# Kernel optimization log

Hardware: AMD Instinct MI355X
Metric: run time of the kernel (lower is better)

The kernel has to match this reference:

```python
import jax, jax.numpy as jnp
import numpy as np

DIM = 256
KEY_DIM = 16
NUM_HEADS = 8
ATTN_RATIO = 4
RES = (32, 32)
N = RES[0] * RES[1]            # 1024 tokens
D = ATTN_RATIO * KEY_DIM       # 64 per-head value dim
DH = D * NUM_HEADS             # 512
H_QKV = DH + 2 * KEY_DIM * NUM_HEADS  # 768
BATCH = 32
EPS = 1e-5


def _bias_idxs():
    # relative-position offset index table: idx[i,j] = |dr|*W + |dc| (bijective
    # over the res0*res1 unique abs-offset pairs, matching the gather structure)
    r = np.arange(RES[0])
    c = np.arange(RES[1])
    rr, cc = np.meshgrid(r, c, indexing='ij')
    pr = rr.reshape(-1)  # [N]
    pc = cc.reshape(-1)
    dr = np.abs(pr[:, None] - pr[None, :])
    dc = np.abs(pc[:, None] - pc[None, :])
    return jnp.asarray(dr * RES[1] + dc, dtype=jnp.int32)  # [N, N]


def setup_inputs() -> dict:
    key = jax.random.key(0)
    ks = jax.random.split(key, 8)
    s_in = 1.0 / np.sqrt(DIM)
    s_dh = 1.0 / np.sqrt(DH)
    return {
        'x': jax.random.normal(ks[0], (BATCH, N, DIM), jnp.float32),
        'norm_w': jnp.ones((DIM,), jnp.float32),
        'norm_b': jnp.zeros((DIM,), jnp.float32),
        'qkv_w': jax.random.normal(ks[1], (H_QKV, DIM), jnp.float32) * s_in,
        'qkv_b': jnp.zeros((H_QKV,), jnp.float32),
        'proj_w': jax.random.normal(ks[2], (DIM, DH), jnp.float32) * s_dh,
        'proj_b': jnp.zeros((DIM,), jnp.float32),
        'attn_biases': jax.random.normal(ks[3], (NUM_HEADS, RES[0] * RES[1]), jnp.float32) * 0.02,
        'bias_idxs': _bias_idxs(),
    }


def reference(x, norm_w, norm_b, qkv_w, qkv_b, proj_w, proj_b, attn_biases, bias_idxs):
    b, n, _ = x.shape
    scale = KEY_DIM ** -0.5
    # LayerNorm
    mu = jnp.mean(x, axis=-1, keepdims=True)
    var = jnp.mean(jnp.square(x - mu), axis=-1, keepdims=True)
    xn = (x - mu) * jax.lax.rsqrt(var + EPS) * norm_w + norm_b
    # fused qkv projection
    qkv = xn @ qkv_w.T + qkv_b                       # [b, n, H_QKV]
    qkv = qkv.reshape(b, n, NUM_HEADS, 2 * KEY_DIM + D)
    q = qkv[..., :KEY_DIM]                           # [b, n, h, k]
    k = qkv[..., KEY_DIM:2 * KEY_DIM]
    v = qkv[..., 2 * KEY_DIM:]                       # [b, n, h, d]
    # scores + gathered relative-position bias
    bias = attn_biases[:, bias_idxs]                 # [h, n, n]
    attn = jnp.einsum('bnhk,bmhk->bhnm', q, k) * scale + bias
    attn = jax.nn.softmax(attn, axis=-1)
    out = jnp.einsum('bhnm,bmhd->bnhd', attn, v).reshape(b, n, DH)
    return out @ proj_w.T + proj_b                   # [b, n, DIM]
```

## Files before the change

### kernel.cpp

```cpp
#include <hip/hip_runtime.h>
#include <hip/hip_bf16.h>

typedef __bf16 bf16x8 __attribute__((ext_vector_type(8)));
typedef float f32x16 __attribute__((ext_vector_type(16)));
typedef float f32x8 __attribute__((ext_vector_type(8)));
typedef float f32x2 __attribute__((ext_vector_type(2)));
typedef unsigned int u32;

#define MFMA32(a, b, c) __builtin_amdgcn_mfma_f32_32x32x16_bf16((a), (b), (c), 0, 0, 0)

__device__ __forceinline__ f32x16 zero16() {
  f32x16 z;
#pragma unroll
  for (int i = 0; i < 16; ++i) z[i] = 0.f;
  return z;
}

__device__ __forceinline__ unsigned short bfb(float f) {
  __hip_bfloat16 h = __float2bfloat16(f);
  return __builtin_bit_cast(unsigned short, h);
}
__device__ __forceinline__ u32 pk2(float lo, float hi) {
  return (u32)bfb(lo) | ((u32)bfb(hi) << 16);
}
__device__ __forceinline__ u32 pk2h(float lo, float hi) {
  _Float16 a = (_Float16)lo, b = (_Float16)hi;
  return (u32)__builtin_bit_cast(unsigned short, a) |
         ((u32)__builtin_bit_cast(unsigned short, b) << 16);
}
__device__ __forceinline__ bf16x8 ld8(const unsigned short* p) {
  return *reinterpret_cast<const bf16x8*>(p);
}
__device__ __forceinline__ void gld_lds16(const void* g, void* l) {
  __builtin_amdgcn_global_load_lds((const __attribute__((address_space(1))) void*)g,
                                   (__attribute__((address_space(3))) void*)l, 16, 0, 0);
}

__global__ __launch_bounds__(256, 4) void ln_kernel(const float* __restrict__ x,
                                                    const float* __restrict__ nw,
                                                    const float* __restrict__ nb,
                                                    unsigned short* __restrict__ xn) {
  int w = threadIdx.x >> 6, lane = threadIdx.x & 63;
  size_t row = (size_t)blockIdx.x * 4 + w;
  float4 v = reinterpret_cast<const float4*>(x + row * 256)[lane];
  float s = (v.x + v.y) + (v.z + v.w);
  float q = (v.x * v.x + v.y * v.y) + (v.z * v.z + v.w * v.w);
#pragma unroll
  for (int m = 1; m < 64; m <<= 1) {
    s += __shfl_xor(s, m, 64);
    q += __shfl_xor(q, m, 64);
  }
  float mu = s * (1.f / 256.f);
  float var = fmaxf(q * (1.f / 256.f) - mu * mu, 0.f);
  float rs = rsqrtf(var + 1e-5f);
  float4 wv = reinterpret_cast<const float4*>(nw)[lane];
  float4 bv = reinterpret_cast<const float4*>(nb)[lane];
  float o0 = (v.x - mu) * rs * wv.x + bv.x;
  float o1 = (v.y - mu) * rs * wv.y + bv.y;
  float o2 = (v.z - mu) * rs * wv.z + bv.z;
  float o3 = (v.w - mu) * rs * wv.w + bv.w;
  uint2 o = make_uint2(pk2(o0, o1), pk2(o2, o3));
  reinterpret_cast<uint2*>(xn + row * 256)[lane] = o;
}

__global__ __launch_bounds__(256, 4) void wconv_kernel(const float* __restrict__ qkv_w,
                                                       const float* __restrict__ proj_w,
                                                       unsigned short* __restrict__ wq,
                                                       unsigned short* __restrict__ wp) {
  int t = blockIdx.x * 256 + threadIdx.x;
  const int NQ = 49152;
  float4 v;
  unsigned short* dst;
  int idx;
  if (t < NQ) {
    v = reinterpret_cast<const float4*>(qkv_w)[t];
    dst = wq;
    idx = t;
  } else {
    v = reinterpret_cast<const float4*>(proj_w)[t - NQ];
    dst = wp;
    idx = t - NQ;
  }
  uint2 o = make_uint2(pk2(v.x, v.y), pk2(v.z, v.w));
  reinterpret_cast<uint2*>(dst)[idx] = o;
}

__global__ __launch_bounds__(256, 4) void bias_gather(const float* __restrict__ attn_biases,
                                                      const int* __restrict__ bias_idxs,
                                                      unsigned short* __restrict__ biasc) {
  int tt = blockIdx.x * 256 + threadIdx.x;
  int j8 = tt & 3;
  int lane = (tt >> 2) & 63;
  int t = (tt >> 8) & 15;
  int g = (tt >> 12) & 31;
  int h = tt >> 17;
  int q = g * 32 + (lane & 31);
  int lh = lane >> 5;
  int sub = j8 >> 1;
  int rb = (j8 & 1) * 16;
  const int* ir = bias_idxs + q * 1024 + (2 * t + sub) * 32 + 4 * lh + rb;
  int4 i0 = *reinterpret_cast<const int4*>(ir);
  int4 i1 = *reinterpret_cast<const int4*>(ir + 8);
  const float* tb = attn_biases + h * 1024;
  const float L2E = 1.4426950408889634f;
  uint4 o;
  o.x = pk2h(tb[i0.x] * L2E, tb[i0.y] * L2E);
  o.y = pk2h(tb[i0.z] * L2E, tb[i0.w] * L2E);
  o.z = pk2h(tb[i1.x] * L2E, tb[i1.y] * L2E);
  o.w = pk2h(tb[i1.z] * L2E, tb[i1.w] * L2E);
  reinterpret_cast<uint4*>(biasc)[tt] = o;
}

template <int STAGES, int ROWB>
__device__ __forceinline__ void gemm_core(const char* Ag, const char* Bg, char* As, char* Bs,
                                          int m0, int n0, int w, int lane, f32x16 acc[2][2]) {
  int lr = lane & 31, lh = lane >> 5;
  for (int kb = 0; kb < STAGES; ++kb) {
    if (kb) __syncthreads();
#pragma unroll
    for (int i = 0; i < 8; ++i) {
      int ldsoff = (i * 4 + w) * 1024;
      int lflat = ldsoff + lane * 16;
      int row = lflat >> 8;
      int c = (lflat >> 4) & 15;
      int sc_ = (c ^ (row & 7)) << 4;
      gld_lds16(Ag + (size_t)(m0 + row) * ROWB + kb * 256 + sc_, As + ldsoff);
      gld_lds16(Bg + (size_t)(n0 + row) * ROWB + kb * 256 + sc_, Bs + ldsoff);
    }
    asm volatile("s_waitcnt vmcnt(0)" ::: "memory");
    __syncthreads();
    int ra = (w >> 1) * 64 + lr;
    int rb = (w & 1) * 64 + lr;
#pragma unroll
    for (int k16 = 0; k16 < 8; ++k16) {
      bf16x8 af[2], bfr[2];
#pragma unroll
      for (int i = 0; i < 2; ++i) {
        int rowa = ra + i * 32;
        int ca = (((k16 << 1) | lh) ^ (rowa & 7)) << 4;
        af[i] = *reinterpret_cast<const bf16x8*>(As + (rowa << 8) + ca);
        int rowb = rb + i * 32;
        int cb = (((k16 << 1) | lh) ^ (rowb & 7)) << 4;
        bfr[i] = *reinterpret_cast<const bf16x8*>(Bs + (rowb << 8) + cb);
      }
#pragma unroll
      for (int i = 0; i < 2; ++i)
#pragma unroll
        for (int j = 0; j < 2; ++j) acc[i][j] = MFMA32(af[i], bfr[j], acc[i][j]);
    }
  }
}

__global__ __launch_bounds__(256, 2) void qkv_gemm(const unsigned short* __restrict__ xn,
                                                   const unsigned short* __restrict__ wq,
                                                   const float* __restrict__ qkv_b,
                                                   unsigned short* __restrict__ Qb,
                                                   unsigned short* __restrict__ Kb,
                                                   unsigned short* __restrict__ Vt) {
  extern __shared__ char smem[];
  char* As = smem;
  char* Bs = smem + 32768;
  int bid = blockIdx.x;
  int f2 = (bid & 7) * 192 + (bid >> 3);
  int nt = f2 % 6, mt = f2 / 6;
  int tid = threadIdx.x, w = tid >> 6, lane = tid & 63;
  int m0 = mt * 128, n0 = nt * 128;
  f32x16 acc[2][2];
  acc[0][0] = zero16(); acc[0][1] = zero16(); acc[1][0] = zero16(); acc[1][1] = zero16();
  gemm_core<2, 512>((const char*)xn, (const char*)wq, As, Bs, m0, n0, w, lane, acc);
  int lr = lane & 31, lh = lane >> 5;
#pragma unroll
  for (int j = 0; j < 2; ++j) {
    int col = n0 + (w & 1) * 64 + j * 32 + lr;
    int h = col / 96;
    int rr = col - h * 96;
    float bv = qkv_b[col];
#pragma unroll
    for (int i = 0; i < 2; ++i) {
      int rbase = m0 + (w >> 1) * 64 + i * 32 + 4 * lh;
      if (rr < 32) {
        unsigned short* dst0 = (rr < 16) ? Qb : Kb;
        int cc = rr & 15;
#pragma unroll
        for (int r = 0; r < 16; ++r) {
          int n = rbase + (r & 3) + 8 * (r >> 2);
          int b = n >> 10, nn = n & 1023;
          dst0[(((size_t)(b * 8 + h) * 1024 + nn) << 4) + cc] = bfb(acc[i][j][r] + bv);
        }
      } else {
        int d = rr - 32;
#pragma unroll
        for (int g = 0; g < 4; ++g) {
          int n = rbase + 8 * g;
          int b = n >> 10, nn = n & 1023;
          int t = nn >> 5, s0 = nn & 31;
          int s = (s0 & ~12) | ((s0 & 4) << 1) | ((s0 & 8) >> 1);
          size_t addr = ((size_t)(b * 8 + h) << 16) + t * 2048 + (s >> 3) * 512 + d * 8 + (s & 7);
          ushort4 pkv;
          pkv.x = bfb(acc[i][j][4 * g + 0] + bv);
          pkv.y = bfb(acc[i][j][4 * g + 1] + bv);
          pkv.z = bfb(acc[i][j][4 * g + 2] + bv);
          pkv.w = bfb(acc[i][j][4 * g + 3] + bv);
          *reinterpret_cast<ushort4*>(Vt + addr) = pkv;
        }
      }
    }
  }
}

__device__ __forceinline__ void stage_tile(const char* kgB, const char* vgB, char* buf,
                                           int t, int w, int lane) {
  const char* vsrc = vgB + (size_t)t * 8192;
  if (w < 2) {
    gld_lds16(kgB + (size_t)t * 2048 + w * 1024 + lane * 16, buf + w * 1024);
    gld_lds16(vsrc + w * 1024 + lane * 16, buf + 2048 + w * 1024);
    gld_lds16(vsrc + (4 + w) * 1024 + lane * 16, buf + 2048 + (4 + w) * 1024);
  } else {
    gld_lds16(vsrc + w * 1024 + lane * 16, buf + 2048 + w * 1024);
    gld_lds16(vsrc + (4 + w) * 1024 + lane * 16, buf + 2048 + (4 + w) * 1024);
  }
}

__device__ __forceinline__ bf16x8 cvt8(const float* p) {
  f32x8 v;
#pragma unroll
  for (int i = 0; i < 8; ++i) v[i] = p[i];
  return __builtin_convertvector(v, bf16x8);
}

__global__ __launch_bounds__(256, 2) void attn_kernel(const unsigned short* __restrict__ Qb,
                                                      const unsigned short* __restrict__ Kb,
                                                      const unsigned short* __restrict__ Vt,
                                                      const unsigned short* __restrict__ biasc,
                                                      unsigned short* __restrict__ aout) {
  extern __shared__ char smem[];
  int bid = blockIdx.x;
  int f2 = (bid & 7) * 128 + (bid >> 3);
  int qt = f2 & 3, b = (f2 >> 2) & 31, h = f2 >> 7;
  int w = threadIdx.x >> 6, lane = threadIdx.x & 63;
  int lr = lane & 31, lh = lane >> 5;
  int bh = b * 8 + h;
  int q0 = qt * 256 + w * 64 + lr;
  bf16x8 qf0 = ld8(Qb + (((size_t)bh * 1024 + q0) << 4) + lh * 8);
  bf16x8 qf1 = ld8(Qb + (((size_t)bh * 1024 + q0 + 32) << 4) + lh * 8);
  const char* kgB = (const char*)Kb + ((size_t)bh << 15);
  const char* vgB = (const char*)Vt + ((size_t)bh << 17);
  int g0 = qt * 8 + w * 2;
  const char* bgB0 = (const char*)biasc + ((size_t)((h * 32 + g0) * 1024 + lane) << 6);
  const char* bgB1 = bgB0 + ((size_t)1024 << 6);
  f32x16 acc00 = zero16(), acc01 = zero16();
  f32x16 acc10 = zero16(), acc11 = zero16();
  f32x2 ls0 = {0.f, 0.f}, ls1 = {0.f, 0.f};
  const float SC = 0.25f * 1.4426950408889634f;

  stage_tile(kgB, vgB, smem, 0, w, lane);

  for (int t = 0; t < 16; ++t) {
    char* cur = smem + (t & 1) * 10240;
    char* nxt = smem + ((t + 1) & 1) * 10240;
    asm volatile("s_waitcnt vmcnt(0)" ::: "memory");
    __builtin_amdgcn_sched_barrier(0);
    __builtin_amdgcn_s_barrier();
    __builtin_amdgcn_sched_barrier(0);
    const char* bp0 = bgB0 + (size_t)t * 4096;
    const char* bp1 = bgB1 + (size_t)t * 4096;
    uint4 b00 = *reinterpret_cast<const uint4*>(bp0);
    uint4 b01 = *reinterpret_cast<const uint4*>(bp0 + 16);
    uint4 b02 = *reinterpret_cast<const uint4*>(bp0 + 32);
    uint4 b03 = *reinterpret_cast<const uint4*>(bp0 + 48);
    uint4 b10 = *reinterpret_cast<const uint4*>(bp1);
    uint4 b11 = *reinterpret_cast<const uint4*>(bp1 + 16);
    uint4 b12 = *reinterpret_cast<const uint4*>(bp1 + 32);
    uint4 b13 = *reinterpret_cast<const uint4*>(bp1 + 48);
    bf16x8 kf0 = *reinterpret_cast<const bf16x8*>(cur + lr * 32 + lh * 16);
    bf16x8 kf1 = *reinterpret_cast<const bf16x8*>(cur + 1024 + lr * 32 + lh * 16);
    const char* Vs = cur + 2048;
    bf16x8 va00 = *reinterpret_cast<const bf16x8*>(Vs + lh * 1024 + lr * 16);
    bf16x8 va10 = *reinterpret_cast<const bf16x8*>(Vs + (2 + lh) * 1024 + lr * 16);
    bf16x8 va01 = *reinterpret_cast<const bf16x8*>(Vs + lh * 1024 + 512 + lr * 16);
    bf16x8 va11 = *reinterpret_cast<const bf16x8*>(Vs + (2 + lh) * 1024 + 512 + lr * 16);
    bf16x8 vb00 = *reinterpret_cast<const bf16x8*>(Vs + 4096 + lh * 1024 + lr * 16);
    bf16x8 vb10 = *reinterpret_cast<const bf16x8*>(Vs + 4096 + (2 + lh) * 1024 + lr * 16);
    bf16x8 vb01 = *reinterpret_cast<const bf16x8*>(Vs + 4096 + lh * 1024 + 512 + lr * 16);
    bf16x8 vb11 = *reinterpret_cast<const bf16x8*>(Vs + 4096 + (2 + lh) * 1024 + 512 + lr * 16);
    stage_tile(kgB, vgB, nxt, t + 1, w, lane);
    __builtin_amdgcn_sched_barrier(0);
    __builtin_amdgcn_s_setprio(1);
    f32x16 stA0 = MFMA32(kf0, qf0, zero16());
    f32x16 stB0 = MFMA32(kf1, qf0, zero16());
    f32x16 stA1 = MFMA32(kf0, qf1, zero16());
    f32x16 stB1 = MFMA32(kf1, qf1, zero16());
    union BB { uint4 u[2]; _Float16 hh[16]; };
    {
      BB bb; bb.u[0] = b00; bb.u[1] = b01;
      float p[16];
#pragma unroll
      for (int r = 0; r < 16; ++r)
        p[r] = __builtin_amdgcn_exp2f(fmaf(stA0[r], SC, (float)bb.hh[r]));
      bf16x8 a0 = cvt8(p), a1 = cvt8(p + 8);
      acc00 = MFMA32(a0, va00, acc00);
      acc01 = MFMA32(a0, va01, acc01);
      acc00 = MFMA32(a1, va10, acc00);
      acc01 = MFMA32(a1, va11, acc01);
#pragma unroll
      for (int i = 0; i < 8; ++i) { f32x2 e = {p[2 * i], p[2 * i + 1]}; ls0 += e; }
    }
    {
      BB bb; bb.u[0] = b02; bb.u[1] = b03;
      float p[16];
#pragma unroll
      for (int r = 0; r < 16; ++r)
        p[r] = __builtin_amdgcn_exp2f(fmaf(stB0[r], SC, (float)bb.hh[r]));
      bf16x8 a0 = cvt8(p), a1 = cvt8(p + 8);
      acc00 = MFMA32(a0, vb00, acc00);
      acc01 = MFMA32(a0, vb01, acc01);
      acc00 = MFMA32(a1, vb10, acc00);
      acc01 = MFMA32(a1, vb11, acc01);
#pragma unroll
      for (int i = 0; i < 8; ++i) { f32x2 e = {p[2 * i], p[2 * i + 1]}; ls0 += e; }
    }
    {
      BB bb; bb.u[0] = b10; bb.u[1] = b11;
      float p[16];
#pragma unroll
      for (int r = 0; r < 16; ++r)
        p[r] = __builtin_amdgcn_exp2f(fmaf(stA1[r], SC, (float)bb.hh[r]));
      bf16x8 a0 = cvt8(p), a1 = cvt8(p + 8);
      acc10 = MFMA32(a0, va00, acc10);
      acc11 = MFMA32(a0, va01, acc11);
      acc10 = MFMA32(a1, va10, acc10);
      acc11 = MFMA32(a1, va11, acc11);
#pragma unroll
      for (int i = 0; i < 8; ++i) { f32x2 e = {p[2 * i], p[2 * i + 1]}; ls1 += e; }
    }
    {
      BB bb; bb.u[0] = b12; bb.u[1] = b13;
      float p[16];
#pragma unroll
      for (int r = 0; r < 16; ++r)
        p[r] = __builtin_amdgcn_exp2f(fmaf(stB1[r], SC, (float)bb.hh[r]));
      bf16x8 a0 = cvt8(p), a1 = cvt8(p + 8);
      acc10 = MFMA32(a0, vb00, acc10);
      acc11 = MFMA32(a0, vb01, acc11);
      acc10 = MFMA32(a1, vb10, acc10);
      acc11 = MFMA32(a1, vb11, acc11);
#pragma unroll
      for (int i = 0; i < 8; ++i) { f32x2 e = {p[2 * i], p[2 * i + 1]}; ls1 += e; }
    }
    __builtin_amdgcn_s_setprio(0);
  }

  float l0 = ls0[0] + ls0[1];
  float s0 = l0 + __shfl_xor(l0, 32, 64);
  float inv0 = 1.f / s0;
  float l1 = ls1[0] + ls1[1];
  float s1 = l1 + __shfl_xor(l1, 32, 64);
  float inv1 = 1.f / s1;
  size_t ob0 = (((size_t)b << 10) + qt * 256 + w * 64) * 512 + h * 64;
  size_t ob1 = ob0 + (size_t)32 * 512;
#pragma unroll
  for (int r = 0; r < 16; ++r) {
    int qrow = (r & 3) + 8 * (r >> 2) + 4 * lh;
    float c0 = __shfl(inv0, qrow, 64);
    aout[ob0 + (size_t)qrow * 512 + lr] = bfb(acc00[r] * c0);
    aout[ob0 + (size_t)qrow * 512 + 32 + lr] = bfb(acc01[r] * c0);
    float c1 = __shfl(inv1, qrow, 64);
    aout[ob1 + (size_t)qrow * 512 + lr] = bfb(acc10[r] * c1);
    aout[ob1 + (size_t)qrow * 512 + 32 + lr] = bfb(acc11[r] * c1);
  }
}

__global__ __launch_bounds__(256, 2) void proj_gemm(const unsigned short* __restrict__ Ain,
                                                    const unsigned short* __restrict__ wp,
                                                    const float* __restrict__ proj_b,
                                                    float* __restrict__ out) {
  extern __shared__ char smem[];
  char* As = smem;
  char* Bs = smem + 32768;
  int bid = blockIdx.x;
  int f2 = (bid & 7) * 64 + (bid >> 3);
  int nt = f2 & 1, mt = f2 >> 1;
  int tid = threadIdx.x, w = tid >> 6, lane = tid & 63;
  int m0 = mt * 128, n0 = nt * 128;
  f32x16 acc[2][2];
  acc[0][0] = zero16(); acc[0][1] = zero16(); acc[1][0] = zero16(); acc[1][1] = zero16();
  gemm_core<4, 1024>((const char*)Ain, (const char*)wp, As, Bs, m0, n0, w, lane, acc);
  int lr = lane & 31, lh = lane >> 5;
#pragma unroll
  for (int j = 0; j < 2; ++j) {
    int col = n0 + (w & 1) * 64 + j * 32 + lr;
    float pbv = proj_b[col];
#pragma unroll
    for (int i = 0; i < 2; ++i) {
      int rbase = m0 + (w >> 1) * 64 + i * 32 + 4 * lh;
#pragma unroll
      for (int r = 0; r < 16; ++r) {
        int n = rbase + (r & 3) + 8 * (r >> 2);
        out[(size_t)n * 256 + col] = acc[i][j][r] + pbv;
      }
    }
  }
}

extern "C" void kernel_launch(void* const* d_in, const int* in_sizes, int n_in,
                              void* d_out, int out_size, void* d_ws, size_t ws_size,
                              hipStream_t stream) {
  const float* x = (const float*)d_in[0];
  const float* norm_w = (const float*)d_in[1];
  const float* norm_b = (const float*)d_in[2];
  const float* qkv_w = (const float*)d_in[3];
  const float* qkv_b = (const float*)d_in[4];
  const float* proj_w = (const float*)d_in[5];
  const float* proj_b = (const float*)d_in[6];
  const float* attn_biases = (const float*)d_in[7];
  const int* bias_idxs = (const int*)d_in[8];
  float* out = (float*)d_out;
  char* ws = (char*)d_ws;
  unsigned short* xn = (unsigned short*)(ws + 0);
  unsigned short* wq = (unsigned short*)(ws + 16777216);
  unsigned short* wp = (unsigned short*)(ws + 17170432);
  unsigned short* Qb = (unsigned short*)(ws + 17432576);
  unsigned short* Kb = (unsigned short*)(ws + 25821184);
  unsigned short* Vt = (unsigned short*)(ws + 34209792);
  unsigned short* biasc = (unsigned short*)(ws + 67764224);
  unsigned short* aout = (unsigned short*)(ws + 84541440);

  ln_kernel<<<8192, 256, 0, stream>>>(x, norm_w, norm_b, xn);
  wconv_kernel<<<320, 256, 0, stream>>>(qkv_w, proj_w, wq, wp);
  bias_gather<<<4096, 256, 0, stream>>>(attn_biases, bias_idxs, biasc);
  qkv_gemm<<<1536, 256, 65536, stream>>>(xn, wq, qkv_b, Qb, Kb, Vt);
  attn_kernel<<<1024, 256, 20480, stream>>>(Qb, Kb, Vt, biasc, aout);
  proj_gemm<<<512, 256, 65536, stream>>>(aout, wp, proj_b, out);
}
```

Baseline: 130.0 us.

## Merge prep kernels into one launch and widen attention blocks to 512 query rows

Three preprocessing kernels (layernorm, weight conversion, bias gather) become a single kernel that picks its work by block index, removing two launches and the gaps between them. The attention kernel now runs 512 threads (8 waves) per block, covering 512 queries per (batch, head) instead of 256. Each K/V tile staged in shared memory is therefore reused by twice as many waves, and each wave issues fewer global-to-LDS loads. The cost is larger blocks that may lower scheduling flexibility, and half as many attention blocks to spread across the CUs.

```diff
diff --git a/kernel.cpp b/kernel.cpp
--- a/kernel.cpp
+++ b/kernel.cpp
@@ -36,79 +36,75 @@
                                    (__attribute__((address_space(3))) void*)l, 16, 0, 0);
 }
 
-__global__ __launch_bounds__(256, 4) void ln_kernel(const float* __restrict__ x,
-                                                    const float* __restrict__ nw,
-                                                    const float* __restrict__ nb,
-                                                    unsigned short* __restrict__ xn) {
-  int w = threadIdx.x >> 6, lane = threadIdx.x & 63;
-  size_t row = (size_t)blockIdx.x * 4 + w;
-  float4 v = reinterpret_cast<const float4*>(x + row * 256)[lane];
-  float s = (v.x + v.y) + (v.z + v.w);
-  float q = (v.x * v.x + v.y * v.y) + (v.z * v.z + v.w * v.w);
-#pragma unroll
-  for (int m = 1; m < 64; m <<= 1) {
-    s += __shfl_xor(s, m, 64);
-    q += __shfl_xor(q, m, 64);
-  }
-  float mu = s * (1.f / 256.f);
-  float var = fmaxf(q * (1.f / 256.f) - mu * mu, 0.f);
-  float rs = rsqrtf(var + 1e-5f);
-  float4 wv = reinterpret_cast<const float4*>(nw)[lane];
-  float4 bv = reinterpret_cast<const float4*>(nb)[lane];
-  float o0 = (v.x - mu) * rs * wv.x + bv.x;
-  float o1 = (v.y - mu) * rs * wv.y + bv.y;
-  float o2 = (v.z - mu) * rs * wv.z + bv.z;
-  float o3 = (v.w - mu) * rs * wv.w + bv.w;
-  uint2 o = make_uint2(pk2(o0, o1), pk2(o2, o3));
-  reinterpret_cast<uint2*>(xn + row * 256)[lane] = o;
-}
-
-__global__ __launch_bounds__(256, 4) void wconv_kernel(const float* __restrict__ qkv_w,
-                                                       const float* __restrict__ proj_w,
-                                                       unsigned short* __restrict__ wq,
-                                                       unsigned short* __restrict__ wp) {
-  int t = blockIdx.x * 256 + threadIdx.x;
-  const int NQ = 49152;
-  float4 v;
-  unsigned short* dst;
-  int idx;
-  if (t < NQ) {
-    v = reinterpret_cast<const float4*>(qkv_w)[t];
-    dst = wq;
-    idx = t;
+__global__ __launch_bounds__(256, 4) void prep_kernel(
+    const float* __restrict__ x, const float* __restrict__ nw, const float* __restrict__ nb,
+    unsigned short* __restrict__ xn, const float* __restrict__ qkv_w,
+    const float* __restrict__ proj_w, unsigned short* __restrict__ wq,
+    unsigned short* __restrict__ wp, const float* __restrict__ attn_biases,
+    const int* __restrict__ bias_idxs, unsigned short* __restrict__ biasc) {
+  int bid = blockIdx.x;
+  if (bid < 8192) {
+    int w = threadIdx.x >> 6, lane = threadIdx.x & 63;
+    size_t row = (size_t)bid * 4 + w;
+    float4 v = reinterpret_cast<const float4*>(x + row * 256)[lane];
+    float s = (v.x + v.y) + (v.z + v.w);
+    float q = (v.x * v.x + v.y * v.y) + (v.z * v.z + v.w * v.w);
+#pragma unroll
+    for (int m = 1; m < 64; m <<= 1) {
+      s += __shfl_xor(s, m, 64);
+      q += __shfl_xor(q, m, 64);
+    }
+    float mu = s * (1.f / 256.f);
+    float var = fmaxf(q * (1.f / 256.f) - mu * mu, 0.f);
+    float rs = rsqrtf(var + 1e-5f);
+    float4 wv = reinterpret_cast<const float4*>(nw)[lane];
+    float4 bv = reinterpret_cast<const float4*>(nb)[lane];
+    float o0 = (v.x - mu) * rs * wv.x + bv.x;
+    float o1 = (v.y - mu) * rs * wv.y + bv.y;
+    float o2 = (v.z - mu) * rs * wv.z + bv.z;
+    float o3 = (v.w - mu) * rs * wv.w + bv.w;
+    uint2 o = make_uint2(pk2(o0, o1), pk2(o2, o3));
+    reinterpret_cast<uint2*>(xn + row * 256)[lane] = o;
+  } else if (bid < 8512) {
+    int t = (bid - 8192) * 256 + threadIdx.x;
+    const int NQ = 49152;
+    float4 v;
+    unsigned short* dst;
+    int idx;
+    if (t < NQ) {
+      v = reinterpret_cast<const float4*>(qkv_w)[t];
+      dst = wq;
+      idx = t;
+    } else {
+      v = reinterpret_cast<const float4*>(proj_w)[t - NQ];
+      dst = wp;
+      idx = t - NQ;
+    }
+    uint2 o = make_uint2(pk2(v.x, v.y), pk2(v.z, v.w));
+    reinterpret_cast<uint2*>(dst)[idx] = o;
   } else {
-    v = reinterpret_cast<const float4*>(proj_w)[t - NQ];
-    dst = wp;
-    idx = t - NQ;
-  }
-  uint2 o = make_uint2(pk2(v.x, v.y), pk2(v.z, v.w));
-  reinterpret_cast<uint2*>(dst)[idx] = o;
-}
-
-__global__ __launch_bounds__(256, 4) void bias_gather(const float* __restrict__ attn_biases,
-                                                      const int* __restrict__ bias_idxs,
-                                                      unsigned short* __restrict__ biasc) {
-  int tt = blockIdx.x * 256 + threadIdx.x;
-  int j8 = tt & 3;
-  int lane = (tt >> 2) & 63;
-  int t = (tt >> 8) & 15;
-  int g = (tt >> 12) & 31;
-  int h = tt >> 17;
-  int q = g * 32 + (lane & 31);
-  int lh = lane >> 5;
-  int sub = j8 >> 1;
-  int rb = (j8 & 1) * 16;
-  const int* ir = bias_idxs + q * 1024 + (2 * t + sub) * 32 + 4 * lh + rb;
-  int4 i0 = *reinterpret_cast<const int4*>(ir);
-  int4 i1 = *reinterpret_cast<const int4*>(ir + 8);
-  const float* tb = attn_biases + h * 1024;
-  const float L2E = 1.4426950408889634f;
-  uint4 o;
-  o.x = pk2h(tb[i0.x] * L2E, tb[i0.y] * L2E);
-  o.y = pk2h(tb[i0.z] * L2E, tb[i0.w] * L2E);
-  o.z = pk2h(tb[i1.x] * L2E, tb[i1.y] * L2E);
-  o.w = pk2h(tb[i1.z] * L2E, tb[i1.w] * L2E);
-  reinterpret_cast<uint4*>(biasc)[tt] = o;
+    int tt = (bid - 8512) * 256 + threadIdx.x;
+    int j8 = tt & 3;
+    int lane = (tt >> 2) & 63;
+    int t = (tt >> 8) & 15;
+    int g = (tt >> 12) & 31;
+    int h = tt >> 17;
+    int q = g * 32 + (lane & 31);
+    int lh = lane >> 5;
+    int sub = j8 >> 1;
+    int rb = (j8 & 1) * 16;
+    const int* ir = bias_idxs + q * 1024 + (2 * t + sub) * 32 + 4 * lh + rb;
+    int4 i0 = *reinterpret_cast<const int4*>(ir);
+    int4 i1 = *reinterpret_cast<const int4*>(ir + 8);
+    const float* tb = attn_biases + h * 1024;
+    const float L2E = 1.4426950408889634f;
+    uint4 o;
+    o.x = pk2h(tb[i0.x] * L2E, tb[i0.y] * L2E);
+    o.y = pk2h(tb[i0.z] * L2E, tb[i0.w] * L2E);
+    o.z = pk2h(tb[i1.x] * L2E, tb[i1.y] * L2E);
+    o.w = pk2h(tb[i1.z] * L2E, tb[i1.w] * L2E);
+    reinterpret_cast<uint4*>(biasc)[tt] = o;
+  }
 }
 
 template <int STAGES, int ROWB>
@@ -208,17 +204,11 @@
   }
 }
 
-__device__ __forceinline__ void stage_tile(const char* kgB, const char* vgB, char* buf,
-                                           int t, int w, int lane) {
+__device__ __forceinline__ void stage_tile8(const char* kgB, const char* vgB, char* buf,
+                                            int t, int w, int lane) {
   const char* vsrc = vgB + (size_t)t * 8192;
-  if (w < 2) {
-    gld_lds16(kgB + (size_t)t * 2048 + w * 1024 + lane * 16, buf + w * 1024);
-    gld_lds16(vsrc + w * 1024 + lane * 16, buf + 2048 + w * 1024);
-    gld_lds16(vsrc + (4 + w) * 1024 + lane * 16, buf + 2048 + (4 + w) * 1024);
-  } else {
-    gld_lds16(vsrc + w * 1024 + lane * 16, buf + 2048 + w * 1024);
-    gld_lds16(vsrc + (4 + w) * 1024 + lane * 16, buf + 2048 + (4 + w) * 1024);
-  }
+  gld_lds16(vsrc + w * 1024 + lane * 16, buf + 2048 + w * 1024);
+  if (w < 2) gld_lds16(kgB + (size_t)t * 2048 + w * 1024 + lane * 16, buf + w * 1024);
 }
 
 __device__ __forceinline__ bf16x8 cvt8(const float* p) {
@@ -228,24 +218,25 @@
   return __builtin_convertvector(v, bf16x8);
 }
 
-__global__ __launch_bounds__(256, 2) void attn_kernel(const unsigned short* __restrict__ Qb,
+__global__ __launch_bounds__(512, 2) void attn_kernel(const unsigned short* __restrict__ Qb,
                                                       const unsigned short* __restrict__ Kb,
                                                       const unsigned short* __restrict__ Vt,
                                                       const unsigned short* __restrict__ biasc,
                                                       unsigned short* __restrict__ aout) {
   extern __shared__ char smem[];
   int bid = blockIdx.x;
-  int f2 = (bid & 7) * 128 + (bid >> 3);
-  int qt = f2 & 3, b = (f2 >> 2) & 31, h = f2 >> 7;
-  int w = threadIdx.x >> 6, lane = threadIdx.x & 63;
+  int f2 = (bid & 7) * 64 + (bid >> 3);
+  int half = f2 & 1, b = (f2 >> 1) & 31, h = f2 >> 6;
+  int tid = threadIdx.x;
+  int w = tid >> 6, lane = tid & 63;
   int lr = lane & 31, lh = lane >> 5;
   int bh = b * 8 + h;
-  int q0 = qt * 256 + w * 64 + lr;
+  int q0 = half * 512 + w * 64 + lr;
   bf16x8 qf0 = ld8(Qb + (((size_t)bh * 1024 + q0) << 4) + lh * 8);
   bf16x8 qf1 = ld8(Qb + (((size_t)bh * 1024 + q0 + 32) << 4) + lh * 8);
   const char* kgB = (const char*)Kb + ((size_t)bh << 15);
   const char* vgB = (const char*)Vt + ((size_t)bh << 17);
-  int g0 = qt * 8 + w * 2;
+  int g0 = half * 16 + w * 2;
   const char* bgB0 = (const char*)biasc + ((size_t)((h * 32 + g0) * 1024 + lane) << 6);
   const char* bgB1 = bgB0 + ((size_t)1024 << 6);
   f32x16 acc00 = zero16(), acc01 = zero16();
@@ -253,7 +244,7 @@
   f32x2 ls0 = {0.f, 0.f}, ls1 = {0.f, 0.f};
   const float SC = 0.25f * 1.4426950408889634f;
 
-  stage_tile(kgB, vgB, smem, 0, w, lane);
+  stage_tile8(kgB, vgB, smem, 0, w, lane);
 
   for (int t = 0; t < 16; ++t) {
     char* cur = smem + (t & 1) * 10240;
@@ -283,7 +274,7 @@
     bf16x8 vb10 = *reinterpret_cast<const bf16x8*>(Vs + 4096 + (2 + lh) * 1024 + lr * 16);
     bf16x8 vb01 = *reinterpret_cast<const bf16x8*>(Vs + 4096 + lh * 1024 + 512 + lr * 16);
     bf16x8 vb11 = *reinterpret_cast<const bf16x8*>(Vs + 4096 + (2 + lh) * 1024 + 512 + lr * 16);
-    stage_tile(kgB, vgB, nxt, t + 1, w, lane);
+    stage_tile8(kgB, vgB, nxt, t + 1, w, lane);
     __builtin_amdgcn_sched_barrier(0);
     __builtin_amdgcn_s_setprio(1);
     f32x16 stA0 = MFMA32(kf0, qf0, zero16());
@@ -356,7 +347,7 @@
   float l1 = ls1[0] + ls1[1];
   float s1 = l1 + __shfl_xor(l1, 32, 64);
   float inv1 = 1.f / s1;
-  size_t ob0 = (((size_t)b << 10) + qt * 256 + w * 64) * 512 + h * 64;
+  size_t ob0 = (((size_t)b << 10) + half * 512 + w * 64) * 512 + h * 64;
   size_t ob1 = ob0 + (size_t)32 * 512;
 #pragma unroll
   for (int r = 0; r < 16; ++r) {
@@ -425,10 +416,9 @@
   unsigned short* biasc = (unsigned short*)(ws + 67764224);
   unsigned short* aout = (unsigned short*)(ws + 84541440);
 
-  ln_kernel<<<8192, 256, 0, stream>>>(x, norm_w, norm_b, xn);
-  wconv_kernel<<<320, 256, 0, stream>>>(qkv_w, proj_w, wq, wp);
-  bias_gather<<<4096, 256, 0, stream>>>(attn_biases, bias_idxs, biasc);
+  prep_kernel<<<12608, 256, 0, stream>>>(x, norm_w, norm_b, xn, qkv_w, proj_w, wq, wp,
+                                         attn_biases, bias_idxs, biasc);
   qkv_gemm<<<1536, 256, 65536, stream>>>(xn, wq, qkv_b, Qb, Kb, Vt);
-  attn_kernel<<<1024, 256, 20480, stream>>>(Qb, Kb, Vt, biasc, aout);
+  attn_kernel<<<512, 512, 20480, stream>>>(Qb, Kb, Vt, biasc, aout);
   proj_gemm<<<512, 256, 65536, stream>>>(aout, wp, proj_b, out);
 }
```

Measured after the change: 137.5 us. 1.06x slower.
